# Optimization experiments

Hardware: AMD Instinct MI355X
Metric: run time of the kernel (lower is better)

The kernel has to match this reference:

```python
import jax, jax.numpy as jnp
import numpy as np

N_NODES = 100_000
N_EDGES = 3_200_000
F_IN, F_HID, F_OUT = 128, 128, 128
MLP_HID, MLP_OUT = 256, 64


def setup_inputs() -> dict:
    key = jax.random.key(0)
    ks = jax.random.split(key, 11)
    def w(k, shape):
        fan_in = shape[0]
        return jax.random.normal(k, shape, jnp.float32) / jnp.sqrt(jnp.float32(fan_in))
    return {
        'x':   jax.random.normal(ks[0], (N_NODES, F_IN), jnp.float32),
        'src': jax.random.randint(ks[1], (N_EDGES,), 0, N_NODES, jnp.int32),
        'dst': jax.random.randint(ks[2], (N_EDGES,), 0, N_NODES, jnp.int32),
        'w1':  w(ks[3], (F_IN, F_HID)),  'b1': jnp.zeros((F_HID,), jnp.float32),
        'w2':  w(ks[4], (F_HID, F_OUT)), 'b2': jnp.zeros((F_OUT,), jnp.float32),
        'wm1': w(ks[5], (F_OUT, MLP_HID)), 'bm1': jnp.zeros((MLP_HID,), jnp.float32),
        'wm2': w(ks[6], (MLP_HID, MLP_OUT)), 'bm2': jnp.zeros((MLP_OUT,), jnp.float32),
    }


def reference(x, src, dst, w1, b1, w2, b2, wm1, bm1, wm2, bm2):
    n = x.shape[0]
    ones = jnp.ones(src.shape[0], x.dtype)
    # DGL GraphConv norm='both': clamp degrees to >=1, symmetric D^-1/2 A D^-1/2
    out_norm = jnp.clip(jax.ops.segment_sum(ones, src, num_segments=n), 1.0) ** -0.5
    in_norm = jnp.clip(jax.ops.segment_sum(ones, dst, num_segments=n), 1.0) ** -0.5

    def gconv(h, w, b):
        msg = (h * out_norm[:, None])[src]                       # [E, F] gather
        agg = jax.ops.segment_sum(msg, dst, num_segments=n)      # [N, F] scatter-add
        return (agg * in_norm[:, None]) @ w + b

    h = jax.nn.relu(gconv(x, w1, b1))   # conv1 + relu (dropout is identity in eval)
    h = jax.nn.relu(gconv(h, w2, b2))   # conv2 + relu
    h = jax.nn.relu(h @ wm1 + bm1)      # MLP hidden layer
    return h @ wm2 + bm2                # MLP output (no final activation)
```

## Files before the change

kernel.cpp:

```cpp
#include <hip/hip_runtime.h>
#include <hip/hip_bf16.h>
#include <cstdint>

__device__ __forceinline__ unsigned short f2b(float f) {
    union { float f; unsigned int i; } v; v.f = f;
    unsigned int i = v.i;
    unsigned int r = (i + 0x7FFFu + ((i >> 16) & 1u)) >> 16;
    return (unsigned short)r;
}
__device__ __forceinline__ float b2f_lo(unsigned int p) {
    union { unsigned int i; float f; } v; v.i = p << 16; return v.f;
}
__device__ __forceinline__ float b2f_hi(unsigned int p) {
    union { unsigned int i; float f; } v; v.i = p & 0xFFFF0000u; return v.f;
}
__device__ __forceinline__ unsigned int pack2(float a, float b) {
    return (unsigned int)f2b(a) | ((unsigned int)f2b(b) << 16);
}

typedef __attribute__((__ext_vector_type__(8))) __bf16 bf16x8;
typedef __attribute__((__ext_vector_type__(4))) float  f32x4;

#define N_NODES 100000
#define N_EDGES 3200000
#define NBUCK   800
#define BSZ     125
#define NCHUNK  256
#define CHUNK   12500
#define BCAP    4864

__global__ __launch_bounds__(1024)
void k_scatter(const int* __restrict__ src, const int* __restrict__ dst,
               int* __restrict__ gcurA, int* __restrict__ gcurB,
               unsigned* __restrict__ pairs, unsigned short* __restrict__ keysB,
               int E) {
    __shared__ int hA[NBUCK], hB[NBUCK], baA[NBUCK], baB[NBUCK], lcA[NBUCK], lcB[NBUCK];
    int t = threadIdx.x, b = blockIdx.x;
    int lo = b * CHUNK, hi = min(lo + CHUNK, E);
    for (int j = t; j < NBUCK; j += 1024) { hA[j] = 0; hB[j] = 0; }
    __syncthreads();
    for (int i = lo + t; i < hi; i += 1024) {
        atomicAdd(&hA[dst[i] / BSZ], 1);
        atomicAdd(&hB[src[i] / BSZ], 1);
    }
    __syncthreads();
    for (int j = t; j < NBUCK; j += 1024) {
        baA[j] = hA[j] ? (j * BCAP + atomicAdd(&gcurA[j], hA[j])) : 0;
        lcA[j] = 0;
        baB[j] = hB[j] ? (j * BCAP + atomicAdd(&gcurB[j], hB[j])) : 0;
        lcB[j] = 0;
    }
    __syncthreads();
    for (int i = lo + t; i < hi; i += 1024) {
        int s = src[i], d = dst[i];
        int bA = d / BSZ;
        int l  = atomicAdd(&lcA[bA], 1);
        pairs[baA[bA] + l] = ((unsigned)(d - bA * BSZ) << 17) | (unsigned)s;
        int bB = s / BSZ;
        int l2 = atomicAdd(&lcB[bB], 1);
        keysB[baB[bB] + l2] = (unsigned short)(s - bB * BSZ);
    }
}

__global__ __launch_bounds__(512)
void k_build2(const unsigned* __restrict__ pairs, const unsigned short* __restrict__ keys,
              const int* __restrict__ bcntA, const int* __restrict__ bcntB,
              int* __restrict__ offsets, int* __restrict__ ends,
              float* __restrict__ in_norm, int* __restrict__ esrc,
              const float4* __restrict__ x4, float* __restrict__ out_norm,
              uint2* __restrict__ xs,
              const float* __restrict__ w1, const float* __restrict__ w2,
              const float* __restrict__ wm1, const float* __restrict__ wm2,
              unsigned short* __restrict__ t1, unsigned short* __restrict__ t2,
              unsigned short* __restrict__ tm1, unsigned short* __restrict__ tm2) {
    __shared__ int el[BCAP];
    __shared__ int hist[128], scan[128], curs[128];
    __shared__ float onl[BSZ];
    int b = blockIdx.x, t = threadIdx.x;

    if (b < NBUCK) {
        int node0 = b * BSZ;
        int bstart = b * BCAP;
        int cnt = bcntA[b];
        int bend = bstart + cnt;
        if (t < 128) hist[t] = 0;
        __syncthreads();
        for (int i = bstart + t; i < bend; i += 512)
            atomicAdd(&hist[pairs[i] >> 17], 1);
        __syncthreads();
        if (t < 128) scan[t] = hist[t];
        __syncthreads();
        for (int d = 1; d < 128; d <<= 1) {
            int v = (t < 128 && t >= d) ? scan[t - d] : 0;
            __syncthreads();
            if (t < 128) scan[t] += v;
            __syncthreads();
        }
        if (t < BSZ) {
            int excl = scan[t] - hist[t];
            offsets[node0 + t] = bstart + excl;
            ends[node0 + t]    = bstart + scan[t];
            in_norm[node0 + t] = rsqrtf((float)max(hist[t], 1));
            curs[t] = excl;
        }
        __syncthreads();
        for (int i = bstart + t; i < bend; i += 512) {
            unsigned p = pairs[i];
            int d = (int)(p >> 17);
            int l = atomicAdd(&curs[d], 1);
            el[l] = (int)(p & 0x1FFFFu);
        }
        __syncthreads();
        int wv = t >> 6, lane = t & 63;
        const int INF = 0x7FFFFFFF;
        for (int n = wv; n < BSZ; n += 8) {
            int len = hist[n];
            if (len <= 1) continue;
            int base = scan[n] - len;
            if (len <= 64) {
                int v0 = (lane < len) ? el[base + lane] : INF;
#pragma unroll
                for (int k = 2; k <= 64; k <<= 1) {
#pragma unroll
                    for (int d = 32; d > 0; d >>= 1) {
                        if (d >= k) continue;
                        int w0 = __shfl_xor(v0, d, 64);
                        bool up = ((lane & k) == 0);
                        bool lower = ((lane & d) == 0);
                        v0 = (lower == up) ? min(v0, w0) : max(v0, w0);
                    }
                }
                if (lane < len) el[base + lane] = v0;
            } else {
                int v0 = (lane < len) ? el[base + lane] : INF;
                int v1 = (64 + lane < len) ? el[base + 64 + lane] : INF;
#pragma unroll
                for (int k = 2; k <= 128; k <<= 1) {
#pragma unroll
                    for (int d = 64; d > 0; d >>= 1) {
                        if (d >= k) continue;
                        if (d == 64) {
                            int a = min(v0, v1), bb = max(v0, v1);
                            v0 = a; v1 = bb;
                        } else {
                            int w0 = __shfl_xor(v0, d, 64);
                            int w1 = __shfl_xor(v1, d, 64);
                            bool up0 = ((lane & k) == 0);
                            bool up1 = (((64 + lane) & k) == 0);
                            bool lower = ((lane & d) == 0);
                            v0 = (lower == up0) ? min(v0, w0) : max(v0, w0);
                            v1 = (lower == up1) ? min(v1, w1) : max(v1, w1);
                        }
                    }
                }
                if (lane < len) el[base + lane] = v0;
                if (64 + lane < len) el[base + 64 + lane] = v1;
            }
        }
        __syncthreads();
        for (int i = t; i < cnt; i += 512) esrc[bstart + i] = el[i];
    } else {
        int bb = b - NBUCK;
        {
            int gid = bb * 512 + t;
            if (gid < 81920) {
                const float* w; unsigned short* tt; int Nn, idx;
                if (gid < 16384)       { w = w1;  tt = t1;  Nn = 128; idx = gid; }
                else if (gid < 32768)  { w = w2;  tt = t2;  Nn = 128; idx = gid - 16384; }
                else if (gid < 65536)  { w = wm1; tt = tm1; Nn = 256; idx = gid - 32768; }
                else                   { w = wm2; tt = tm2; Nn = 64;  idx = gid - 65536; }
                int K = (gid < 65536) ? 128 : 256;
                int k = idx / Nn, n = idx - k * Nn;
                tt[(size_t)n * K + k] = f2b(w[idx]);
            }
        }
        int node0 = bb * BSZ;
        int bstart = bb * BCAP;
        int bend = bstart + bcntB[bb];
        if (t < 128) hist[t] = 0;
        __syncthreads();
        for (int i = bstart + t; i < bend; i += 512)
            atomicAdd(&hist[keys[i]], 1);
        __syncthreads();
        if (t < BSZ) {
            float on = rsqrtf((float)max(hist[t], 1));
            onl[t] = on;
            out_norm[node0 + t] = on;
        }
        __syncthreads();
        size_t base4 = (size_t)node0 * 32;
        for (int i = t; i < BSZ * 32; i += 512) {
            float on = onl[i >> 5];
            float4 v = x4[base4 + i];
            uint2 o;
            o.x = pack2(v.x * on, v.y * on);
            o.y = pack2(v.z * on, v.w * on);
            xs[base4 + i] = o;
        }
    }
}

#define AGG_ADD(p)                                                              \
        a0 += b2f_lo(p.x); a1 += b2f_hi(p.x);                                   \
        a2 += b2f_lo(p.y); a3 += b2f_hi(p.y);                                   \
        a4 += b2f_lo(p.z); a5 += b2f_hi(p.z);                                   \
        a6 += b2f_lo(p.w); a7 += b2f_hi(p.w);

#define AGG_NODE_BODY(node)                                                     \
    int lo = offsets[node], hi = ends[node];                                    \
    float a0 = 0.f, a1 = 0.f, a2 = 0.f, a3 = 0.f,                               \
          a4 = 0.f, a5 = 0.f, a6 = 0.f, a7 = 0.f;                               \
    int k = lo + g;                                                             \
    for (; k + 12 < hi; k += 16) {                                              \
        int s0 = esrc[k];                                                       \
        int s1 = esrc[k + 4];                                                   \
        int s2 = esrc[k + 8];                                                   \
        int s3 = esrc[k + 12];                                                  \
        uint4 p0 = feat[(size_t)s0 * 16 + c];                                   \
        uint4 p1 = feat[(size_t)s1 * 16 + c];                                   \
        uint4 p2 = feat[(size_t)s2 * 16 + c];                                   \
        uint4 p3 = feat[(size_t)s3 * 16 + c];                                   \
        AGG_ADD(p0) AGG_ADD(p1) AGG_ADD(p2) AGG_ADD(p3)                         \
    }                                                                           \
    for (; k < hi; k += 4) {                                                    \
        int s = esrc[k];                                                        \
        uint4 p = feat[(size_t)s * 16 + c];                                     \
        AGG_ADD(p)                                                              \
    }                                                                           \
    a0 += __shfl_xor(a0, 16, 64); a0 += __shfl_xor(a0, 32, 64);                 \
    a1 += __shfl_xor(a1, 16, 64); a1 += __shfl_xor(a1, 32, 64);                 \
    a2 += __shfl_xor(a2, 16, 64); a2 += __shfl_xor(a2, 32, 64);                 \
    a3 += __shfl_xor(a3, 16, 64); a3 += __shfl_xor(a3, 32, 64);                 \
    a4 += __shfl_xor(a4, 16, 64); a4 += __shfl_xor(a4, 32, 64);                 \
    a5 += __shfl_xor(a5, 16, 64); a5 += __shfl_xor(a5, 32, 64);                 \
    a6 += __shfl_xor(a6, 16, 64); a6 += __shfl_xor(a6, 32, 64);                 \
    a7 += __shfl_xor(a7, 16, 64); a7 += __shfl_xor(a7, 32, 64);

__global__ __launch_bounds__(256, 8)
void k_conv(const int* __restrict__ offsets, const int* __restrict__ ends,
            const int* __restrict__ esrc,
            const uint4* __restrict__ feat, const float* __restrict__ in_norm,
            const unsigned short* __restrict__ WT, const float* __restrict__ bias,
            const float* __restrict__ row_scale, unsigned short* __restrict__ C,
            int N) {
    __shared__ __align__(16) unsigned short A[32][136];
    int wv = threadIdx.x >> 6, lane = threadIdx.x & 63;
    int row0 = blockIdx.x * 32;
    int g = lane >> 4, c = lane & 15;

    for (int i = 0; i < 8; ++i) {
        int nl = wv * 8 + i;
        int node = row0 + nl;
        AGG_NODE_BODY(node)
        if (g == 0) {
            float inn = in_norm[node];
            uint4 o;
            o.x = pack2(a0 * inn, a1 * inn);
            o.y = pack2(a2 * inn, a3 * inn);
            o.z = pack2(a4 * inn, a5 * inn);
            o.w = pack2(a6 * inn, a7 * inn);
            *(uint4*)&A[nl][c * 8] = o;
        }
    }
    __syncthreads();

    int m = lane & 15, q = lane >> 4;
    const unsigned short* b0 = WT + (size_t)(wv * 32 + m) * 128 + q * 8;
    const unsigned short* b1 = b0 + (size_t)16 * 128;
    f32x4 acc00 = {0.f, 0.f, 0.f, 0.f}, acc10 = {0.f, 0.f, 0.f, 0.f};
    f32x4 acc01 = {0.f, 0.f, 0.f, 0.f}, acc11 = {0.f, 0.f, 0.f, 0.f};
#pragma unroll
    for (int k = 0; k < 128; k += 32) {
        bf16x8 bf0 = *(const bf16x8*)(b0 + k);
        bf16x8 bf1 = *(const bf16x8*)(b1 + k);
        bf16x8 af0 = *(const bf16x8*)&A[m][q * 8 + k];
        bf16x8 af1 = *(const bf16x8*)&A[16 + m][q * 8 + k];
        acc00 = __builtin_amdgcn_mfma_f32_16x16x32_bf16(af0, bf0, acc00, 0, 0, 0);
        acc10 = __builtin_amdgcn_mfma_f32_16x16x32_bf16(af1, bf0, acc10, 0, 0, 0);
        acc01 = __builtin_amdgcn_mfma_f32_16x16x32_bf16(af0, bf1, acc01, 0, 0, 0);
        acc11 = __builtin_amdgcn_mfma_f32_16x16x32_bf16(af1, bf1, acc11, 0, 0, 0);
    }
    __syncthreads();

    int col0 = wv * 32 + m;
    int col1 = col0 + 16;
    float bc0 = bias[col0], bc1 = bias[col1];
#pragma unroll
    for (int r = 0; r < 4; r++) {
        int rl = q * 4 + r;
        int rr = row0 + rl, rr1 = rr + 16;
        float v00 = fmaxf(acc00[r] + bc0, 0.f);
        float v10 = fmaxf(acc10[r] + bc0, 0.f);
        float v01 = fmaxf(acc01[r] + bc1, 0.f);
        float v11 = fmaxf(acc11[r] + bc1, 0.f);
        float s0 = row_scale[rr], s1 = row_scale[rr1];
        v00 *= s0; v01 *= s0; v10 *= s1; v11 *= s1;
        A[rl][col0]      = f2b(v00);
        A[rl][col1]      = f2b(v01);
        A[rl + 16][col0] = f2b(v10);
        A[rl + 16][col1] = f2b(v11);
    }
    __syncthreads();
#pragma unroll
    for (int it = 0; it < 2; ++it) {
        int idx = it * 256 + (int)threadIdx.x;
        int row = idx >> 4, seg = idx & 15;
        uint4 v = *(const uint4*)&A[row][seg * 8];
        *(uint4*)&C[(size_t)(row0 + row) * 128 + seg * 8] = v;
    }
}

__global__ __launch_bounds__(256, 8)
void k_conv2_mlp(const int* __restrict__ offsets, const int* __restrict__ ends,
                 const int* __restrict__ esrc,
                 const uint4* __restrict__ feat, const float* __restrict__ in_norm,
                 const unsigned short* __restrict__ WT2, const float* __restrict__ b2,
                 const unsigned short* __restrict__ WTM1, const float* __restrict__ bm1,
                 const unsigned short* __restrict__ WTM2, const float* __restrict__ bm2,
                 float* __restrict__ out, int N) {
    __shared__ __align__(16) unsigned short smem[8704];
    unsigned short (*H1)[136] = (unsigned short(*)[136])(smem);
    unsigned short (*A)[136]  = (unsigned short(*)[136])(smem + 4352);
    unsigned short (*H2)[136] = (unsigned short(*)[136])(smem + 4352);

    int wv = threadIdx.x >> 6, lane = threadIdx.x & 63;
    int row0 = blockIdx.x * 32;
    int g = lane >> 4, c = lane & 15;

    for (int i = 0; i < 8; ++i) {
        int nl = wv * 8 + i;
        int node = row0 + nl;
        AGG_NODE_BODY(node)
        if (g == 0) {
            float inn = in_norm[node];
            uint4 o;
            o.x = pack2(a0 * inn, a1 * inn);
            o.y = pack2(a2 * inn, a3 * inn);
            o.z = pack2(a4 * inn, a5 * inn);
            o.w = pack2(a6 * inn, a7 * inn);
            *(uint4*)&A[nl][c * 8] = o;
        }
    }
    __syncthreads();

    int m = lane & 15, q = lane >> 4;

    {
        const unsigned short* bb0 = WT2 + (size_t)(wv * 32 + m) * 128 + q * 8;
        const unsigned short* bb1 = bb0 + (size_t)16 * 128;
        f32x4 acc00 = {0.f, 0.f, 0.f, 0.f}, acc10 = {0.f, 0.f, 0.f, 0.f};
        f32x4 acc01 = {0.f, 0.f, 0.f, 0.f}, acc11 = {0.f, 0.f, 0.f, 0.f};
#pragma unroll
        for (int k = 0; k < 128; k += 32) {
            bf16x8 bf0 = *(const bf16x8*)(bb0 + k);
            bf16x8 bf1 = *(const bf16x8*)(bb1 + k);
            bf16x8 af0 = *(const bf16x8*)&A[m][q * 8 + k];
            bf16x8 af1 = *(const bf16x8*)&A[16 + m][q * 8 + k];
            acc00 = __builtin_amdgcn_mfma_f32_16x16x32_bf16(af0, bf0, acc00, 0, 0, 0);
            acc10 = __builtin_amdgcn_mfma_f32_16x16x32_bf16(af1, bf0, acc10, 0, 0, 0);
            acc01 = __builtin_amdgcn_mfma_f32_16x16x32_bf16(af0, bf1, acc01, 0, 0, 0);
            acc11 = __builtin_amdgcn_mfma_f32_16x16x32_bf16(af1, bf1, acc11, 0, 0, 0);
        }
        int col0 = wv * 32 + m;
        int col1 = col0 + 16;
        float bc0 = b2[col0], bc1 = b2[col1];
#pragma unroll
        for (int r = 0; r < 4; r++) {
            int rl = q * 4 + r;
            H1[rl][col0]      = f2b(fmaxf(acc00[r] + bc0, 0.f));
            H1[rl][col1]      = f2b(fmaxf(acc01[r] + bc1, 0.f));
            H1[rl + 16][col0] = f2b(fmaxf(acc10[r] + bc0, 0.f));
            H1[rl + 16][col1] = f2b(fmaxf(acc11[r] + bc1, 0.f));
        }
    }
    __syncthreads();

    f32x4 macc0 = {0.f, 0.f, 0.f, 0.f}, macc1 = {0.f, 0.f, 0.f, 0.f};
    int colo = wv * 16 + m;
    const unsigned short* bp2 = WTM2 + (size_t)colo * 256 + q * 8;
#pragma unroll
    for (int half = 0; half < 2; ++half) {
#pragma unroll
        for (int cb = 0; cb < 2; cb++) {
            int colh = half * 128 + wv * 32 + cb * 16 + m;
            const unsigned short* bp = WTM1 + (size_t)colh * 128 + q * 8;
            f32x4 acc0 = {0.f, 0.f, 0.f, 0.f};
            f32x4 acc1 = {0.f, 0.f, 0.f, 0.f};
#pragma unroll
            for (int s = 0; s < 4; s++) {
                bf16x8 bfr = *(const bf16x8*)(bp + s * 32);
                bf16x8 ha0 = *(const bf16x8*)&H1[m][s * 32 + q * 8];
                bf16x8 ha1 = *(const bf16x8*)&H1[m + 16][s * 32 + q * 8];
                acc0 = __builtin_amdgcn_mfma_f32_16x16x32_bf16(ha0, bfr, acc0, 0, 0, 0);
                acc1 = __builtin_amdgcn_mfma_f32_16x16x32_bf16(ha1, bfr, acc1, 0, 0, 0);
            }
            float bc = bm1[colh];
            int cl = colh & 127;
#pragma unroll
            for (int r = 0; r < 4; r++) {
                H2[q * 4 + r][cl]      = f2b(fmaxf(acc0[r] + bc, 0.f));
                H2[q * 4 + r + 16][cl] = f2b(fmaxf(acc1[r] + bc, 0.f));
            }
        }
        __syncthreads();
#pragma unroll
        for (int s = 0; s < 4; s++) {
            bf16x8 bfr = *(const bf16x8*)(bp2 + half * 128 + s * 32);
            bf16x8 ha0 = *(const bf16x8*)&H2[m][s * 32 + q * 8];
            bf16x8 ha1 = *(const bf16x8*)&H2[m + 16][s * 32 + q * 8];
            macc0 = __builtin_amdgcn_mfma_f32_16x16x32_bf16(ha0, bfr, macc0, 0, 0, 0);
            macc1 = __builtin_amdgcn_mfma_f32_16x16x32_bf16(ha1, bfr, macc1, 0, 0, 0);
        }
        __syncthreads();
    }

    float* OS = (float*)smem;
    float bc = bm2[colo];
#pragma unroll
    for (int r = 0; r < 4; r++) {
        OS[(q * 4 + r) * 64 + colo]        = macc0[r] + bc;
        OS[(q * 4 + r + 16) * 64 + colo]   = macc1[r] + bc;
    }
    __syncthreads();
#pragma unroll
    for (int it = 0; it < 2; ++it) {
        int idx = it * 256 + (int)threadIdx.x;
        int row = idx >> 4, seg = idx & 15;
        f32x4 v = *(const f32x4*)&OS[row * 64 + seg * 4];
        __builtin_nontemporal_store(v, (f32x4*)&out[(size_t)(row0 + row) * 64 + seg * 4]);
    }
}

extern "C" void kernel_launch(void* const* d_in, const int* in_sizes, int n_in,
                              void* d_out, int out_size, void* d_ws, size_t ws_size,
                              hipStream_t stream) {
    const float* x    = (const float*)d_in[0];
    const int*   src  = (const int*)d_in[1];
    const int*   dst  = (const int*)d_in[2];
    const float* w1   = (const float*)d_in[3];
    const float* b1   = (const float*)d_in[4];
    const float* w2   = (const float*)d_in[5];
    const float* b2   = (const float*)d_in[6];
    const float* wm1  = (const float*)d_in[7];
    const float* bm1  = (const float*)d_in[8];
    const float* wm2  = (const float*)d_in[9];
    const float* bm2  = (const float*)d_in[10];

    const int N = N_NODES;
    const int E = N_EDGES;

    char* p = (char*)d_ws;
    auto alloc = [&](size_t bytes) -> void* {
        void* r = (void*)p;
        p += (bytes + 255) & ~(size_t)255;
        return r;
    };
    int*   gcurA   = (int*)alloc(NBUCK * 4);
    int*   gcurB   = (int*)alloc(NBUCK * 4);
    int*   offsets = (int*)alloc((size_t)N * 4);
    int*   ends    = (int*)alloc((size_t)N * 4);
    float* out_norm = (float*)alloc((size_t)N * 4);
    float* in_norm  = (float*)alloc((size_t)N * 4);
    int*   esrc     = (int*)alloc((size_t)NBUCK * BCAP * 4);
    unsigned int* bufA = (unsigned int*)alloc((size_t)N * 128 * 2);
    unsigned int* bufB = (unsigned int*)alloc((size_t)N * 128 * 2);
    unsigned int* bufC = (unsigned int*)alloc((size_t)N * 128 * 2);
    unsigned short* wt1  = (unsigned short*)alloc(128 * 128 * 2);
    unsigned short* wt2  = (unsigned short*)alloc(128 * 128 * 2);
    unsigned short* wtm1 = (unsigned short*)alloc(256 * 128 * 2);
    unsigned short* wtm2 = (unsigned short*)alloc(64 * 256 * 2);
    (void)ws_size; (void)n_in; (void)in_sizes; (void)out_size;

    unsigned*       pairs = (unsigned*)bufB;
    unsigned short* keysB = (unsigned short*)bufC;

    (void)hipMemsetAsync(gcurA, 0, (size_t)((char*)gcurB - (char*)gcurA) + NBUCK * 4, stream);

    const int TB = 256;
    k_scatter<<<dim3(NCHUNK), dim3(1024), 0, stream>>>(src, dst, gcurA, gcurB,
                                                       pairs, keysB, E);
    k_build2<<<dim3(2 * NBUCK), dim3(512), 0, stream>>>(
        pairs, keysB, gcurA, gcurB, offsets, ends, in_norm, esrc,
        (const float4*)x, out_norm, (uint2*)bufA,
        w1, w2, wm1, wm2, wt1, wt2, wtm1, wtm2);

    k_conv<<<dim3(N / 32), dim3(TB), 0, stream>>>(
        offsets, ends, esrc, (const uint4*)bufA, in_norm, wt1, b1, out_norm,
        (unsigned short*)bufC, N);

    k_conv2_mlp<<<dim3(N / 32), dim3(TB), 0, stream>>>(
        offsets, ends, esrc, (const uint4*)bufC, in_norm, wt2, b2, wtm1, bm1, wtm2, bm2,
        (float*)d_out, N);
}
```

Baseline: 487.3 us.

## Use persistent blocks with atomic tile tickets for build and conv kernels

Converts k_build2, k_conv and k_conv2_mlp into persistent-grid kernels. Each block claims tile indices from a global atomic ticket counter until the work runs out, instead of launching one block per tile. It also doubles the number of scatter chunks (512 chunks of 6250 edges). The intent is to balance uneven per-tile gather work across CUs and cut block launch overhead. The cost is an atomic plus a barrier per tile, and the ticket counters now share the zeroed workspace.

```diff
diff --git a/kernel.cpp b/kernel.cpp
--- a/kernel.cpp
+++ b/kernel.cpp
@@ -25,9 +25,11 @@
 #define N_EDGES 3200000
 #define NBUCK   800
 #define BSZ     125
-#define NCHUNK  256
-#define CHUNK   12500
+#define NCHUNK  512
+#define CHUNK   6250
 #define BCAP    4864
+#define CONV_GRID  2048
+#define BUILD_GRID 1024
 
 __global__ __launch_bounds__(1024)
 void k_scatter(const int* __restrict__ src, const int* __restrict__ dst,
@@ -72,130 +74,139 @@
               const float* __restrict__ w1, const float* __restrict__ w2,
               const float* __restrict__ wm1, const float* __restrict__ wm2,
               unsigned short* __restrict__ t1, unsigned short* __restrict__ t2,
-              unsigned short* __restrict__ tm1, unsigned short* __restrict__ tm2) {
+              unsigned short* __restrict__ tm1, unsigned short* __restrict__ tm2,
+              int* __restrict__ ticket) {
     __shared__ int el[BCAP];
     __shared__ int hist[128], scan[128], curs[128];
     __shared__ float onl[BSZ];
-    int b = blockIdx.x, t = threadIdx.x;
-
-    if (b < NBUCK) {
-        int node0 = b * BSZ;
-        int bstart = b * BCAP;
-        int cnt = bcntA[b];
-        int bend = bstart + cnt;
-        if (t < 128) hist[t] = 0;
-        __syncthreads();
-        for (int i = bstart + t; i < bend; i += 512)
-            atomicAdd(&hist[pairs[i] >> 17], 1);
-        __syncthreads();
-        if (t < 128) scan[t] = hist[t];
-        __syncthreads();
-        for (int d = 1; d < 128; d <<= 1) {
-            int v = (t < 128 && t >= d) ? scan[t - d] : 0;
-            __syncthreads();
-            if (t < 128) scan[t] += v;
-            __syncthreads();
-        }
-        if (t < BSZ) {
-            int excl = scan[t] - hist[t];
-            offsets[node0 + t] = bstart + excl;
-            ends[node0 + t]    = bstart + scan[t];
-            in_norm[node0 + t] = rsqrtf((float)max(hist[t], 1));
-            curs[t] = excl;
-        }
-        __syncthreads();
-        for (int i = bstart + t; i < bend; i += 512) {
-            unsigned p = pairs[i];
-            int d = (int)(p >> 17);
-            int l = atomicAdd(&curs[d], 1);
-            el[l] = (int)(p & 0x1FFFFu);
-        }
-        __syncthreads();
-        int wv = t >> 6, lane = t & 63;
-        const int INF = 0x7FFFFFFF;
-        for (int n = wv; n < BSZ; n += 8) {
-            int len = hist[n];
-            if (len <= 1) continue;
-            int base = scan[n] - len;
-            if (len <= 64) {
-                int v0 = (lane < len) ? el[base + lane] : INF;
-#pragma unroll
-                for (int k = 2; k <= 64; k <<= 1) {
-#pragma unroll
-                    for (int d = 32; d > 0; d >>= 1) {
-                        if (d >= k) continue;
-                        int w0 = __shfl_xor(v0, d, 64);
-                        bool up = ((lane & k) == 0);
-                        bool lower = ((lane & d) == 0);
-                        v0 = (lower == up) ? min(v0, w0) : max(v0, w0);
-                    }
-                }
-                if (lane < len) el[base + lane] = v0;
-            } else {
-                int v0 = (lane < len) ? el[base + lane] : INF;
-                int v1 = (64 + lane < len) ? el[base + 64 + lane] : INF;
-#pragma unroll
-                for (int k = 2; k <= 128; k <<= 1) {
-#pragma unroll
-                    for (int d = 64; d > 0; d >>= 1) {
-                        if (d >= k) continue;
-                        if (d == 64) {
-                            int a = min(v0, v1), bb = max(v0, v1);
-                            v0 = a; v1 = bb;
-                        } else {
+    __shared__ int s_tile;
+    int t = threadIdx.x;
+
+    while (true) {
+        if (t == 0) s_tile = atomicAdd(ticket, 1);
+        __syncthreads();
+        int b = s_tile;
+        if (b >= 2 * NBUCK) return;
+
+        if (b < NBUCK) {
+            int node0 = b * BSZ;
+            int bstart = b * BCAP;
+            int cnt = bcntA[b];
+            int bend = bstart + cnt;
+            if (t < 128) hist[t] = 0;
+            __syncthreads();
+            for (int i = bstart + t; i < bend; i += 512)
+                atomicAdd(&hist[pairs[i] >> 17], 1);
+            __syncthreads();
+            if (t < 128) scan[t] = hist[t];
+            __syncthreads();
+            for (int d = 1; d < 128; d <<= 1) {
+                int v = (t < 128 && t >= d) ? scan[t - d] : 0;
+                __syncthreads();
+                if (t < 128) scan[t] += v;
+                __syncthreads();
+            }
+            if (t < BSZ) {
+                int excl = scan[t] - hist[t];
+                offsets[node0 + t] = bstart + excl;
+                ends[node0 + t]    = bstart + scan[t];
+                in_norm[node0 + t] = rsqrtf((float)max(hist[t], 1));
+                curs[t] = excl;
+            }
+            __syncthreads();
+            for (int i = bstart + t; i < bend; i += 512) {
+                unsigned p = pairs[i];
+                int d = (int)(p >> 17);
+                int l = atomicAdd(&curs[d], 1);
+                el[l] = (int)(p & 0x1FFFFu);
+            }
+            __syncthreads();
+            int wv = t >> 6, lane = t & 63;
+            const int INF = 0x7FFFFFFF;
+            for (int n = wv; n < BSZ; n += 8) {
+                int len = hist[n];
+                if (len <= 1) continue;
+                int base = scan[n] - len;
+                if (len <= 64) {
+                    int v0 = (lane < len) ? el[base + lane] : INF;
+#pragma unroll
+                    for (int k = 2; k <= 64; k <<= 1) {
+#pragma unroll
+                        for (int d = 32; d > 0; d >>= 1) {
+                            if (d >= k) continue;
                             int w0 = __shfl_xor(v0, d, 64);
-                            int w1 = __shfl_xor(v1, d, 64);
-                            bool up0 = ((lane & k) == 0);
-                            bool up1 = (((64 + lane) & k) == 0);
+                            bool up = ((lane & k) == 0);
                             bool lower = ((lane & d) == 0);
-                            v0 = (lower == up0) ? min(v0, w0) : max(v0, w0);
-                            v1 = (lower == up1) ? min(v1, w1) : max(v1, w1);
+                            v0 = (lower == up) ? min(v0, w0) : max(v0, w0);
                         }
                     }
+                    if (lane < len) el[base + lane] = v0;
+                } else {
+                    int v0 = (lane < len) ? el[base + lane] : INF;
+                    int v1 = (64 + lane < len) ? el[base + 64 + lane] : INF;
+#pragma unroll
+                    for (int k = 2; k <= 128; k <<= 1) {
+#pragma unroll
+                        for (int d = 64; d > 0; d >>= 1) {
+                            if (d >= k) continue;
+                            if (d == 64) {
+                                int a = min(v0, v1), bb = max(v0, v1);
+                                v0 = a; v1 = bb;
+                            } else {
+                                int w0 = __shfl_xor(v0, d, 64);
+                                int w1 = __shfl_xor(v1, d, 64);
+                                bool up0 = ((lane & k) == 0);
+                                bool up1 = (((64 + lane) & k) == 0);
+                                bool lower = ((lane & d) == 0);
+                                v0 = (lower == up0) ? min(v0, w0) : max(v0, w0);
+                                v1 = (lower == up1) ? min(v1, w1) : max(v1, w1);
+                            }
+                        }
+                    }
+                    if (lane < len) el[base + lane] = v0;
+                    if (64 + lane < len) el[base + 64 + lane] = v1;
                 }
-                if (lane < len) el[base + lane] = v0;
-                if (64 + lane < len) el[base + 64 + lane] = v1;
-            }
-        }
-        __syncthreads();
-        for (int i = t; i < cnt; i += 512) esrc[bstart + i] = el[i];
-    } else {
-        int bb = b - NBUCK;
-        {
-            int gid = bb * 512 + t;
-            if (gid < 81920) {
-                const float* w; unsigned short* tt; int Nn, idx;
-                if (gid < 16384)       { w = w1;  tt = t1;  Nn = 128; idx = gid; }
-                else if (gid < 32768)  { w = w2;  tt = t2;  Nn = 128; idx = gid - 16384; }
-                else if (gid < 65536)  { w = wm1; tt = tm1; Nn = 256; idx = gid - 32768; }
-                else                   { w = wm2; tt = tm2; Nn = 64;  idx = gid - 65536; }
-                int K = (gid < 65536) ? 128 : 256;
-                int k = idx / Nn, n = idx - k * Nn;
-                tt[(size_t)n * K + k] = f2b(w[idx]);
-            }
-        }
-        int node0 = bb * BSZ;
-        int bstart = bb * BCAP;
-        int bend = bstart + bcntB[bb];
-        if (t < 128) hist[t] = 0;
-        __syncthreads();
-        for (int i = bstart + t; i < bend; i += 512)
-            atomicAdd(&hist[keys[i]], 1);
-        __syncthreads();
-        if (t < BSZ) {
-            float on = rsqrtf((float)max(hist[t], 1));
-            onl[t] = on;
-            out_norm[node0 + t] = on;
-        }
-        __syncthreads();
-        size_t base4 = (size_t)node0 * 32;
-        for (int i = t; i < BSZ * 32; i += 512) {
-            float on = onl[i >> 5];
-            float4 v = x4[base4 + i];
-            uint2 o;
-            o.x = pack2(v.x * on, v.y * on);
-            o.y = pack2(v.z * on, v.w * on);
-            xs[base4 + i] = o;
+            }
+            __syncthreads();
+            for (int i = t; i < cnt; i += 512) esrc[bstart + i] = el[i];
+        } else {
+            int bb = b - NBUCK;
+            {
+                int gid = bb * 512 + t;
+                if (gid < 81920) {
+                    const float* w; unsigned short* tt; int Nn, idx;
+                    if (gid < 16384)       { w = w1;  tt = t1;  Nn = 128; idx = gid; }
+                    else if (gid < 32768)  { w = w2;  tt = t2;  Nn = 128; idx = gid - 16384; }
+                    else if (gid < 65536)  { w = wm1; tt = tm1; Nn = 256; idx = gid - 32768; }
+                    else                   { w = wm2; tt = tm2; Nn = 64;  idx = gid - 65536; }
+                    int K = (gid < 65536) ? 128 : 256;
+                    int k = idx / Nn, n = idx - k * Nn;
+                    tt[(size_t)n * K + k] = f2b(w[idx]);
+                }
+            }
+            int node0 = bb * BSZ;
+            int bstart = bb * BCAP;
+            int bend = bstart + bcntB[bb];
+            if (t < 128) hist[t] = 0;
+            __syncthreads();
+            for (int i = bstart + t; i < bend; i += 512)
+                atomicAdd(&hist[keys[i]], 1);
+            __syncthreads();
+            if (t < BSZ) {
+                float on = rsqrtf((float)max(hist[t], 1));
+                onl[t] = on;
+                out_norm[node0 + t] = on;
+            }
+            __syncthreads();
+            size_t base4 = (size_t)node0 * 32;
+            for (int i = t; i < BSZ * 32; i += 512) {
+                float on = onl[i >> 5];
+                float4 v = x4[base4 + i];
+                uint2 o;
+                o.x = pack2(v.x * on, v.y * on);
+                o.y = pack2(v.z * on, v.w * on);
+                xs[base4 + i] = o;
+            }
         }
     }
 }
@@ -242,71 +253,79 @@
             const uint4* __restrict__ feat, const float* __restrict__ in_norm,
             const unsigned short* __restrict__ WT, const float* __restrict__ bias,
             const float* __restrict__ row_scale, unsigned short* __restrict__ C,
-            int N) {
+            int* __restrict__ ticket, int ntiles) {
     __shared__ __align__(16) unsigned short A[32][136];
+    __shared__ int s_tile;
     int wv = threadIdx.x >> 6, lane = threadIdx.x & 63;
-    int row0 = blockIdx.x * 32;
     int g = lane >> 4, c = lane & 15;
-
-    for (int i = 0; i < 8; ++i) {
-        int nl = wv * 8 + i;
-        int node = row0 + nl;
-        AGG_NODE_BODY(node)
-        if (g == 0) {
-            float inn = in_norm[node];
-            uint4 o;
-            o.x = pack2(a0 * inn, a1 * inn);
-            o.y = pack2(a2 * inn, a3 * inn);
-            o.z = pack2(a4 * inn, a5 * inn);
-            o.w = pack2(a6 * inn, a7 * inn);
-            *(uint4*)&A[nl][c * 8] = o;
-        }
-    }
-    __syncthreads();
-
     int m = lane & 15, q = lane >> 4;
-    const unsigned short* b0 = WT + (size_t)(wv * 32 + m) * 128 + q * 8;
-    const unsigned short* b1 = b0 + (size_t)16 * 128;
-    f32x4 acc00 = {0.f, 0.f, 0.f, 0.f}, acc10 = {0.f, 0.f, 0.f, 0.f};
-    f32x4 acc01 = {0.f, 0.f, 0.f, 0.f}, acc11 = {0.f, 0.f, 0.f, 0.f};
-#pragma unroll
-    for (int k = 0; k < 128; k += 32) {
-        bf16x8 bf0 = *(const bf16x8*)(b0 + k);
-        bf16x8 bf1 = *(const bf16x8*)(b1 + k);
-        bf16x8 af0 = *(const bf16x8*)&A[m][q * 8 + k];
-        bf16x8 af1 = *(const bf16x8*)&A[16 + m][q * 8 + k];
-        acc00 = __builtin_amdgcn_mfma_f32_16x16x32_bf16(af0, bf0, acc00, 0, 0, 0);
-        acc10 = __builtin_amdgcn_mfma_f32_16x16x32_bf16(af1, bf0, acc10, 0, 0, 0);
-        acc01 = __builtin_amdgcn_mfma_f32_16x16x32_bf16(af0, bf1, acc01, 0, 0, 0);
-        acc11 = __builtin_amdgcn_mfma_f32_16x16x32_bf16(af1, bf1, acc11, 0, 0, 0);
-    }
-    __syncthreads();
-
-    int col0 = wv * 32 + m;
-    int col1 = col0 + 16;
-    float bc0 = bias[col0], bc1 = bias[col1];
-#pragma unroll
-    for (int r = 0; r < 4; r++) {
-        int rl = q * 4 + r;
-        int rr = row0 + rl, rr1 = rr + 16;
-        float v00 = fmaxf(acc00[r] + bc0, 0.f);
-        float v10 = fmaxf(acc10[r] + bc0, 0.f);
-        float v01 = fmaxf(acc01[r] + bc1, 0.f);
-        float v11 = fmaxf(acc11[r] + bc1, 0.f);
-        float s0 = row_scale[rr], s1 = row_scale[rr1];
-        v00 *= s0; v01 *= s0; v10 *= s1; v11 *= s1;
-        A[rl][col0]      = f2b(v00);
-        A[rl][col1]      = f2b(v01);
-        A[rl + 16][col0] = f2b(v10);
-        A[rl + 16][col1] = f2b(v11);
-    }
-    __syncthreads();
-#pragma unroll
-    for (int it = 0; it < 2; ++it) {
-        int idx = it * 256 + (int)threadIdx.x;
-        int row = idx >> 4, seg = idx & 15;
-        uint4 v = *(const uint4*)&A[row][seg * 8];
-        *(uint4*)&C[(size_t)(row0 + row) * 128 + seg * 8] = v;
+
+    while (true) {
+        if (threadIdx.x == 0) s_tile = atomicAdd(ticket, 1);
+        __syncthreads();
+        int tile = s_tile;
+        if (tile >= ntiles) return;
+        int row0 = tile * 32;
+
+        for (int i = 0; i < 8; ++i) {
+            int nl = wv * 8 + i;
+            int node = row0 + nl;
+            AGG_NODE_BODY(node)
+            if (g == 0) {
+                float inn = in_norm[node];
+                uint4 o;
+                o.x = pack2(a0 * inn, a1 * inn);
+                o.y = pack2(a2 * inn, a3 * inn);
+                o.z = pack2(a4 * inn, a5 * inn);
+                o.w = pack2(a6 * inn, a7 * inn);
+                *(uint4*)&A[nl][c * 8] = o;
+            }
+        }
+        __syncthreads();
+
+        const unsigned short* b0 = WT + (size_t)(wv * 32 + m) * 128 + q * 8;
+        const unsigned short* b1 = b0 + (size_t)16 * 128;
+        f32x4 acc00 = {0.f, 0.f, 0.f, 0.f}, acc10 = {0.f, 0.f, 0.f, 0.f};
+        f32x4 acc01 = {0.f, 0.f, 0.f, 0.f}, acc11 = {0.f, 0.f, 0.f, 0.f};
+#pragma unroll
+        for (int k = 0; k < 128; k += 32) {
+            bf16x8 bf0 = *(const bf16x8*)(b0 + k);
+            bf16x8 bf1 = *(const bf16x8*)(b1 + k);
+            bf16x8 af0 = *(const bf16x8*)&A[m][q * 8 + k];
+            bf16x8 af1 = *(const bf16x8*)&A[16 + m][q * 8 + k];
+            acc00 = __builtin_amdgcn_mfma_f32_16x16x32_bf16(af0, bf0, acc00, 0, 0, 0);
+            acc10 = __builtin_amdgcn_mfma_f32_16x16x32_bf16(af1, bf0, acc10, 0, 0, 0);
+            acc01 = __builtin_amdgcn_mfma_f32_16x16x32_bf16(af0, bf1, acc01, 0, 0, 0);
+            acc11 = __builtin_amdgcn_mfma_f32_16x16x32_bf16(af1, bf1, acc11, 0, 0, 0);
+        }
+        __syncthreads();
+
+        int col0 = wv * 32 + m;
+        int col1 = col0 + 16;
+        float bc0 = bias[col0], bc1 = bias[col1];
+#pragma unroll
+        for (int r = 0; r < 4; r++) {
+            int rl = q * 4 + r;
+            int rr = row0 + rl, rr1 = rr + 16;
+            float v00 = fmaxf(acc00[r] + bc0, 0.f);
+            float v10 = fmaxf(acc10[r] + bc0, 0.f);
+            float v01 = fmaxf(acc01[r] + bc1, 0.f);
+            float v11 = fmaxf(acc11[r] + bc1, 0.f);
+            float s0 = row_scale[rr], s1 = row_scale[rr1];
+            v00 *= s0; v01 *= s0; v10 *= s1; v11 *= s1;
+            A[rl][col0]      = f2b(v00);
+            A[rl][col1]      = f2b(v01);
+            A[rl + 16][col0] = f2b(v10);
+            A[rl + 16][col1] = f2b(v11);
+        }
+        __syncthreads();
+#pragma unroll
+        for (int it = 0; it < 2; ++it) {
+            int idx = it * 256 + (int)threadIdx.x;
+            int row = idx >> 4, seg = idx & 15;
+            uint4 v = *(const uint4*)&A[row][seg * 8];
+            *(uint4*)&C[(size_t)(row0 + row) * 128 + seg * 8] = v;
+        }
     }
 }
 
@@ -317,117 +336,124 @@
                  const unsigned short* __restrict__ WT2, const float* __restrict__ b2,
                  const unsigned short* __restrict__ WTM1, const float* __restrict__ bm1,
                  const unsigned short* __restrict__ WTM2, const float* __restrict__ bm2,
-                 float* __restrict__ out, int N) {
+                 float* __restrict__ out, int* __restrict__ ticket, int ntiles) {
     __shared__ __align__(16) unsigned short smem[8704];
+    __shared__ int s_tile;
     unsigned short (*H1)[136] = (unsigned short(*)[136])(smem);
     unsigned short (*A)[136]  = (unsigned short(*)[136])(smem + 4352);
     unsigned short (*H2)[136] = (unsigned short(*)[136])(smem + 4352);
 
     int wv = threadIdx.x >> 6, lane = threadIdx.x & 63;
-    int row0 = blockIdx.x * 32;
     int g = lane >> 4, c = lane & 15;
-
-    for (int i = 0; i < 8; ++i) {
-        int nl = wv * 8 + i;
-        int node = row0 + nl;
-        AGG_NODE_BODY(node)
-        if (g == 0) {
-            float inn = in_norm[node];
-            uint4 o;
-            o.x = pack2(a0 * inn, a1 * inn);
-            o.y = pack2(a2 * inn, a3 * inn);
-            o.z = pack2(a4 * inn, a5 * inn);
-            o.w = pack2(a6 * inn, a7 * inn);
-            *(uint4*)&A[nl][c * 8] = o;
-        }
-    }
-    __syncthreads();
-
     int m = lane & 15, q = lane >> 4;
 
-    {
-        const unsigned short* bb0 = WT2 + (size_t)(wv * 32 + m) * 128 + q * 8;
-        const unsigned short* bb1 = bb0 + (size_t)16 * 128;
-        f32x4 acc00 = {0.f, 0.f, 0.f, 0.f}, acc10 = {0.f, 0.f, 0.f, 0.f};
-        f32x4 acc01 = {0.f, 0.f, 0.f, 0.f}, acc11 = {0.f, 0.f, 0.f, 0.f};
-#pragma unroll
-        for (int k = 0; k < 128; k += 32) {
-            bf16x8 bf0 = *(const bf16x8*)(bb0 + k);
-            bf16x8 bf1 = *(const bf16x8*)(bb1 + k);
-            bf16x8 af0 = *(const bf16x8*)&A[m][q * 8 + k];
-            bf16x8 af1 = *(const bf16x8*)&A[16 + m][q * 8 + k];
-            acc00 = __builtin_amdgcn_mfma_f32_16x16x32_bf16(af0, bf0, acc00, 0, 0, 0);
-            acc10 = __builtin_amdgcn_mfma_f32_16x16x32_bf16(af1, bf0, acc10, 0, 0, 0);
-            acc01 = __builtin_amdgcn_mfma_f32_16x16x32_bf16(af0, bf1, acc01, 0, 0, 0);
-            acc11 = __builtin_amdgcn_mfma_f32_16x16x32_bf16(af1, bf1, acc11, 0, 0, 0);
-        }
-        int col0 = wv * 32 + m;
-        int col1 = col0 + 16;
-        float bc0 = b2[col0], bc1 = b2[col1];
+    while (true) {
+        if (threadIdx.x == 0) s_tile = atomicAdd(ticket, 1);
+        __syncthreads();
+        int tile = s_tile;
+        if (tile >= ntiles) return;
+        int row0 = tile * 32;
+
+        for (int i = 0; i < 8; ++i) {
+            int nl = wv * 8 + i;
+            int node = row0 + nl;
+            AGG_NODE_BODY(node)
+            if (g == 0) {
+                float inn = in_norm[node];
+                uint4 o;
+                o.x = pack2(a0 * inn, a1 * inn);
+                o.y = pack2(a2 * inn, a3 * inn);
+                o.z = pack2(a4 * inn, a5 * inn);
+                o.w = pack2(a6 * inn, a7 * inn);
+                *(uint4*)&A[nl][c * 8] = o;
+            }
+        }
+        __syncthreads();
+
+        {
+            const unsigned short* bb0 = WT2 + (size_t)(wv * 32 + m) * 128 + q * 8;
+            const unsigned short* bb1 = bb0 + (size_t)16 * 128;
+            f32x4 acc00 = {0.f, 0.f, 0.f, 0.f}, acc10 = {0.f, 0.f, 0.f, 0.f};
+            f32x4 acc01 = {0.f, 0.f, 0.f, 0.f}, acc11 = {0.f, 0.f, 0.f, 0.f};
+#pragma unroll
+            for (int k = 0; k < 128; k += 32) {
+                bf16x8 bf0 = *(const bf16x8*)(bb0 + k);
+                bf16x8 bf1 = *(const bf16x8*)(bb1 + k);
+                bf16x8 af0 = *(const bf16x8*)&A[m][q * 8 + k];
+                bf16x8 af1 = *(const bf16x8*)&A[16 + m][q * 8 + k];
+                acc00 = __builtin_amdgcn_mfma_f32_16x16x32_bf16(af0, bf0, acc00, 0, 0, 0);
+                acc10 = __builtin_amdgcn_mfma_f32_16x16x32_bf16(af1, bf0, acc10, 0, 0, 0);
+                acc01 = __builtin_amdgcn_mfma_f32_16x16x32_bf16(af0, bf1, acc01, 0, 0, 0);
+                acc11 = __builtin_amdgcn_mfma_f32_16x16x32_bf16(af1, bf1, acc11, 0, 0, 0);
+            }
+            int col0 = wv * 32 + m;
+            int col1 = col0 + 16;
+            float bc0 = b2[col0], bc1 = b2[col1];
+#pragma unroll
+            for (int r = 0; r < 4; r++) {
+                int rl = q * 4 + r;
+                H1[rl][col0]      = f2b(fmaxf(acc00[r] + bc0, 0.f));
+                H1[rl][col1]      = f2b(fmaxf(acc01[r] + bc1, 0.f));
+                H1[rl + 16][col0] = f2b(fmaxf(acc10[r] + bc0, 0.f));
+                H1[rl + 16][col1] = f2b(fmaxf(acc11[r] + bc1, 0.f));
+            }
+        }
+        __syncthreads();
+
+        f32x4 macc0 = {0.f, 0.f, 0.f, 0.f}, macc1 = {0.f, 0.f, 0.f, 0.f};
+        int colo = wv * 16 + m;
+        const unsigned short* bp2 = WTM2 + (size_t)colo * 256 + q * 8;
+#pragma unroll
+        for (int half = 0; half < 2; ++half) {
+#pragma unroll
+            for (int cb = 0; cb < 2; cb++) {
+                int colh = half * 128 + wv * 32 + cb * 16 + m;
+                const unsigned short* bp = WTM1 + (size_t)colh * 128 + q * 8;
+                f32x4 acc0 = {0.f, 0.f, 0.f, 0.f};
+                f32x4 acc1 = {0.f, 0.f, 0.f, 0.f};
+#pragma unroll
+                for (int s = 0; s < 4; s++) {
+                    bf16x8 bfr = *(const bf16x8*)(bp + s * 32);
+                    bf16x8 ha0 = *(const bf16x8*)&H1[m][s * 32 + q * 8];
+                    bf16x8 ha1 = *(const bf16x8*)&H1[m + 16][s * 32 + q * 8];
+                    acc0 = __builtin_amdgcn_mfma_f32_16x16x32_bf16(ha0, bfr, acc0, 0, 0, 0);
+                    acc1 = __builtin_amdgcn_mfma_f32_16x16x32_bf16(ha1, bfr, acc1, 0, 0, 0);
+                }
+                float bc = bm1[colh];
+                int cl = colh & 127;
+#pragma unroll
+                for (int r = 0; r < 4; r++) {
+                    H2[q * 4 + r][cl]      = f2b(fmaxf(acc0[r] + bc, 0.f));
+                    H2[q * 4 + r + 16][cl] = f2b(fmaxf(acc1[r] + bc, 0.f));
+                }
+            }
+            __syncthreads();
+#pragma unroll
+            for (int s = 0; s < 4; s++) {
+                bf16x8 bfr = *(const bf16x8*)(bp2 + half * 128 + s * 32);
+                bf16x8 ha0 = *(const bf16x8*)&H2[m][s * 32 + q * 8];
+                bf16x8 ha1 = *(const bf16x8*)&H2[m + 16][s * 32 + q * 8];
+                macc0 = __builtin_amdgcn_mfma_f32_16x16x32_bf16(ha0, bfr, macc0, 0, 0, 0);
+                macc1 = __builtin_amdgcn_mfma_f32_16x16x32_bf16(ha1, bfr, macc1, 0, 0, 0);
+            }
+            __syncthreads();
+        }
+
+        float* OS = (float*)smem;
+        float bc = bm2[colo];
 #pragma unroll
         for (int r = 0; r < 4; r++) {
-            int rl = q * 4 + r;
-            H1[rl][col0]      = f2b(fmaxf(acc00[r] + bc0, 0.f));
-            H1[rl][col1]      = f2b(fmaxf(acc01[r] + bc1, 0.f));
-            H1[rl + 16][col0] = f2b(fmaxf(acc10[r] + bc0, 0.f));
-            H1[rl + 16][col1] = f2b(fmaxf(acc11[r] + bc1, 0.f));
-        }
-    }
-    __syncthreads();
-
-    f32x4 macc0 = {0.f, 0.f, 0.f, 0.f}, macc1 = {0.f, 0.f, 0.f, 0.f};
-    int colo = wv * 16 + m;
-    const unsigned short* bp2 = WTM2 + (size_t)colo * 256 + q * 8;
-#pragma unroll
-    for (int half = 0; half < 2; ++half) {
-#pragma unroll
-        for (int cb = 0; cb < 2; cb++) {
-            int colh = half * 128 + wv * 32 + cb * 16 + m;
-            const unsigned short* bp = WTM1 + (size_t)colh * 128 + q * 8;
-            f32x4 acc0 = {0.f, 0.f, 0.f, 0.f};
-            f32x4 acc1 = {0.f, 0.f, 0.f, 0.f};
-#pragma unroll
-            for (int s = 0; s < 4; s++) {
-                bf16x8 bfr = *(const bf16x8*)(bp + s * 32);
-                bf16x8 ha0 = *(const bf16x8*)&H1[m][s * 32 + q * 8];
-                bf16x8 ha1 = *(const bf16x8*)&H1[m + 16][s * 32 + q * 8];
-                acc0 = __builtin_amdgcn_mfma_f32_16x16x32_bf16(ha0, bfr, acc0, 0, 0, 0);
-                acc1 = __builtin_amdgcn_mfma_f32_16x16x32_bf16(ha1, bfr, acc1, 0, 0, 0);
-            }
-            float bc = bm1[colh];
-            int cl = colh & 127;
-#pragma unroll
-            for (int r = 0; r < 4; r++) {
-                H2[q * 4 + r][cl]      = f2b(fmaxf(acc0[r] + bc, 0.f));
-                H2[q * 4 + r + 16][cl] = f2b(fmaxf(acc1[r] + bc, 0.f));
-            }
-        }
-        __syncthreads();
-#pragma unroll
-        for (int s = 0; s < 4; s++) {
-            bf16x8 bfr = *(const bf16x8*)(bp2 + half * 128 + s * 32);
-            bf16x8 ha0 = *(const bf16x8*)&H2[m][s * 32 + q * 8];
-            bf16x8 ha1 = *(const bf16x8*)&H2[m + 16][s * 32 + q * 8];
-            macc0 = __builtin_amdgcn_mfma_f32_16x16x32_bf16(ha0, bfr, macc0, 0, 0, 0);
-            macc1 = __builtin_amdgcn_mfma_f32_16x16x32_bf16(ha1, bfr, macc1, 0, 0, 0);
-        }
-        __syncthreads();
-    }
-
-    float* OS = (float*)smem;
-    float bc = bm2[colo];
-#pragma unroll
-    for (int r = 0; r < 4; r++) {
-        OS[(q * 4 + r) * 64 + colo]        = macc0[r] + bc;
-        OS[(q * 4 + r + 16) * 64 + colo]   = macc1[r] + bc;
-    }
-    __syncthreads();
-#pragma unroll
-    for (int it = 0; it < 2; ++it) {
-        int idx = it * 256 + (int)threadIdx.x;
-        int row = idx >> 4, seg = idx & 15;
-        f32x4 v = *(const f32x4*)&OS[row * 64 + seg * 4];
-        __builtin_nontemporal_store(v, (f32x4*)&out[(size_t)(row0 + row) * 64 + seg * 4]);
+            OS[(q * 4 + r) * 64 + colo]        = macc0[r] + bc;
+            OS[(q * 4 + r + 16) * 64 + colo]   = macc1[r] + bc;
+        }
+        __syncthreads();
+#pragma unroll
+        for (int it = 0; it < 2; ++it) {
+            int idx = it * 256 + (int)threadIdx.x;
+            int row = idx >> 4, seg = idx & 15;
+            f32x4 v = *(const f32x4*)&OS[row * 64 + seg * 4];
+            __builtin_nontemporal_store(v, (f32x4*)&out[(size_t)(row0 + row) * 64 + seg * 4]);
+        }
     }
 }
 
@@ -455,8 +481,9 @@
         p += (bytes + 255) & ~(size_t)255;
         return r;
     };
-    int*   gcurA   = (int*)alloc(NBUCK * 4);
-    int*   gcurB   = (int*)alloc(NBUCK * 4);
+    int*   gcurA   = (int*)alloc((2 * NBUCK + 4) * 4);
+    int*   gcurB   = gcurA + NBUCK;
+    int*   ticks   = gcurA + 2 * NBUCK;
     int*   offsets = (int*)alloc((size_t)N * 4);
     int*   ends    = (int*)alloc((size_t)N * 4);
     float* out_norm = (float*)alloc((size_t)N * 4);
@@ -474,21 +501,21 @@
     unsigned*       pairs = (unsigned*)bufB;
     unsigned short* keysB = (unsigned short*)bufC;
 
-    (void)hipMemsetAsync(gcurA, 0, (size_t)((char*)gcurB - (char*)gcurA) + NBUCK * 4, stream);
+    (void)hipMemsetAsync(gcurA, 0, (2 * NBUCK + 4) * 4, stream);
 
     const int TB = 256;
     k_scatter<<<dim3(NCHUNK), dim3(1024), 0, stream>>>(src, dst, gcurA, gcurB,
                                                        pairs, keysB, E);
-    k_build2<<<dim3(2 * NBUCK), dim3(512), 0, stream>>>(
+    k_build2<<<dim3(BUILD_GRID), dim3(512), 0, stream>>>(
         pairs, keysB, gcurA, gcurB, offsets, ends, in_norm, esrc,
         (const float4*)x, out_norm, (uint2*)bufA,
-        w1, w2, wm1, wm2, wt1, wt2, wtm1, wtm2);
-
-    k_conv<<<dim3(N / 32), dim3(TB), 0, stream>>>(
+        w1, w2, wm1, wm2, wt1, wt2, wtm1, wtm2, ticks);
+
+    k_conv<<<dim3(CONV_GRID), dim3(TB), 0, stream>>>(
         offsets, ends, esrc, (const uint4*)bufA, in_norm, wt1, b1, out_norm,
-        (unsigned short*)bufC, N);
-
-    k_conv2_mlp<<<dim3(N / 32), dim3(TB), 0, stream>>>(
+        (unsigned short*)bufC, ticks + 1, N / 32);
+
+    k_conv2_mlp<<<dim3(CONV_GRID), dim3(TB), 0, stream>>>(
         offsets, ends, esrc, (const uint4*)bufC, in_norm, wt2, b2, wtm1, bm1, wtm2, bm2,
-        (float*)d_out, N);
-}
+        (float*)d_out, ticks + 2, N / 32);
+}
```

Measured after the change: 587.6 us. +20.6%, slower.

## Split conv2 aggregation from fused MLP into separate gather and GEMM kernels

Applied to the files above, without the earlier changes.

The fused conv2+MLP kernel is split in two. A standalone aggregation kernel handles one node per wavefront, four nodes per block, and writes the normalized bf16 aggregate to global memory (reusing bufB). A separate kernel loads those rows into shared memory and runs the three chained matmuls. The aim is finer-grained load balancing of the irregular gather and keeping the MFMA-heavy phase from being held up by gather latency, at the cost of an extra launch and a round trip of a 100k x 128 bf16 buffer through global memory.

```diff
diff --git a/kernel.cpp b/kernel.cpp
--- a/kernel.cpp
+++ b/kernel.cpp
@@ -310,39 +310,51 @@
     }
 }
 
+__global__ __launch_bounds__(256)
+void k_agg(const int* __restrict__ offsets, const int* __restrict__ ends,
+           const int* __restrict__ esrc,
+           const uint4* __restrict__ feat, const float* __restrict__ in_norm,
+           uint4* __restrict__ out, int N) {
+    int node = blockIdx.x * 4 + (threadIdx.x >> 6);
+    if (node >= N) return;
+    int lane = threadIdx.x & 63;
+    int g = lane >> 4, c = lane & 15;
+    AGG_NODE_BODY(node)
+    if (g == 0) {
+        float inn = in_norm[node];
+        uint4 o;
+        o.x = pack2(a0 * inn, a1 * inn);
+        o.y = pack2(a2 * inn, a3 * inn);
+        o.z = pack2(a4 * inn, a5 * inn);
+        o.w = pack2(a6 * inn, a7 * inn);
+        out[(size_t)node * 16 + c] = o;
+    }
+}
+
 __global__ __launch_bounds__(256, 8)
-void k_conv2_mlp(const int* __restrict__ offsets, const int* __restrict__ ends,
-                 const int* __restrict__ esrc,
-                 const uint4* __restrict__ feat, const float* __restrict__ in_norm,
-                 const unsigned short* __restrict__ WT2, const float* __restrict__ b2,
-                 const unsigned short* __restrict__ WTM1, const float* __restrict__ bm1,
-                 const unsigned short* __restrict__ WTM2, const float* __restrict__ bm2,
-                 float* __restrict__ out, int N) {
+void k_mlp3(const uint4* __restrict__ Ag,
+            const unsigned short* __restrict__ WT2, const float* __restrict__ b2,
+            const unsigned short* __restrict__ WTM1, const float* __restrict__ bm1,
+            const unsigned short* __restrict__ WTM2, const float* __restrict__ bm2,
+            float* __restrict__ out) {
     __shared__ __align__(16) unsigned short smem[8704];
     unsigned short (*H1)[136] = (unsigned short(*)[136])(smem);
     unsigned short (*A)[136]  = (unsigned short(*)[136])(smem + 4352);
     unsigned short (*H2)[136] = (unsigned short(*)[136])(smem + 4352);
 
-    int wv = threadIdx.x >> 6, lane = threadIdx.x & 63;
     int row0 = blockIdx.x * 32;
-    int g = lane >> 4, c = lane & 15;
-
-    for (int i = 0; i < 8; ++i) {
-        int nl = wv * 8 + i;
-        int node = row0 + nl;
-        AGG_NODE_BODY(node)
-        if (g == 0) {
-            float inn = in_norm[node];
-            uint4 o;
-            o.x = pack2(a0 * inn, a1 * inn);
-            o.y = pack2(a2 * inn, a3 * inn);
-            o.z = pack2(a4 * inn, a5 * inn);
-            o.w = pack2(a6 * inn, a7 * inn);
-            *(uint4*)&A[nl][c * 8] = o;
-        }
-    }
-    __syncthreads();
-
+    int t = threadIdx.x;
+
+#pragma unroll
+    for (int it = 0; it < 2; ++it) {
+        int idx = it * 256 + t;
+        int row = idx >> 4, seg = idx & 15;
+        uint4 v = Ag[(size_t)(row0 + row) * 16 + seg];
+        *(uint4*)&A[row][seg * 8] = v;
+    }
+    __syncthreads();
+
+    int wv = t >> 6, lane = t & 63;
     int m = lane & 15, q = lane >> 4;
 
     {
@@ -424,7 +436,7 @@
     __syncthreads();
 #pragma unroll
     for (int it = 0; it < 2; ++it) {
-        int idx = it * 256 + (int)threadIdx.x;
+        int idx = it * 256 + t;
         int row = idx >> 4, seg = idx & 15;
         f32x4 v = *(const f32x4*)&OS[row * 64 + seg * 4];
         __builtin_nontemporal_store(v, (f32x4*)&out[(size_t)(row0 + row) * 64 + seg * 4]);
@@ -488,7 +500,9 @@
         offsets, ends, esrc, (const uint4*)bufA, in_norm, wt1, b1, out_norm,
         (unsigned short*)bufC, N);
 
-    k_conv2_mlp<<<dim3(N / 32), dim3(TB), 0, stream>>>(
-        offsets, ends, esrc, (const uint4*)bufC, in_norm, wt2, b2, wtm1, bm1, wtm2, bm2,
-        (float*)d_out, N);
-}
+    k_agg<<<dim3((N + 3) / 4), dim3(TB), 0, stream>>>(
+        offsets, ends, esrc, (const uint4*)bufC, in_norm, (uint4*)bufB, N);
+
+    k_mlp3<<<dim3(N / 32), dim3(TB), 0, stream>>>(
+        (const uint4*)bufB, wt2, b2, wtm1, bm1, wtm2, bm2, (float*)d_out);
+}
```

Measured after the change: 497.1 us. +2.0%, slower.
